# Kernel optimization log

Hardware: AMD Instinct MI355X
Metric: run time of the kernel (lower is better)

## Reference

```python
import jax, jax.numpy as jnp
import numpy as np

TEMPERATURE = 0.07
MSE_WEIGHT = 0.5
SUPCON_WEIGHT = 1.0
EPS = 1e-12  # F.normalize default eps

P_POS = 4000
P_NEG = 4000
NVOX = 32768
FEAT = 128


def setup_inputs() -> dict:
    key = jax.random.key(0)
    k1, k2, k3, k4, k5 = jax.random.split(key, 5)
    Zs = jax.random.normal(k1, (1, FEAT, NVOX), dtype=jnp.float32)
    pos_idx = jax.random.randint(k2, (P_POS,), 0, NVOX, dtype=jnp.int32)
    neg_idx = jax.random.randint(k3, (P_NEG,), 0, NVOX, dtype=jnp.int32)
    feature_diff = jax.random.normal(k4, (1, FEAT, 32, 32, 32), dtype=jnp.float32)
    input_diff = jax.random.normal(k5, (1, FEAT, 32, 32, 32), dtype=jnp.float32)
    return {"Zs": Zs, "pos_idx": pos_idx, "neg_idx": neg_idx,
            "feature_diff": feature_diff, "input_diff": input_diff}


def _l2_normalize_rows(x):
    # F.normalize(x, dim=1): x / max(||x||_2, eps)
    n = jnp.sqrt(jnp.sum(x * x, axis=1, keepdims=True))
    return x / jnp.maximum(n, EPS)


def _supcon_loss(Zs, pos_idx, neg_idx):
    feats = Zs[0].T                                   # [Nvox, F]
    pixels = jnp.concatenate([feats[pos_idx], feats[neg_idx]], axis=0)  # [N, F]
    n = pixels.shape[0]
    labels = jnp.concatenate([jnp.ones((P_POS,), jnp.int32),
                              jnp.zeros((P_NEG,), jnp.int32)])
    pixels = _l2_normalize_rows(pixels)
    dot = jnp.matmul(pixels, pixels.T) / TEMPERATURE  # [N, N]
    dot = _l2_normalize_rows(dot)                     # row-normalize the NxN matrix
    expm = jnp.exp(dot)
    class_mask = (labels[:, None] == labels[None, :]) & ~jnp.eye(n, dtype=bool)
    pos_term = expm * class_mask
    pos_term = jnp.where(pos_term == 0, 1.0, pos_term)
    denom = jnp.sum(expm * ~class_mask, axis=1) - jnp.diagonal(expm)  # [N]
    full_term = jnp.log(pos_term) - jnp.log(denom)[None, :]
    return -(1.0 / n) * jnp.sum(full_term)


def reference(Zs, pos_idx, neg_idx, feature_diff, input_diff):
    supcon = _supcon_loss(Zs, pos_idx, neg_idx)
    mse = jnp.mean((feature_diff - input_diff) ** 2)
    return SUPCON_WEIGHT * supcon + MSE_WEIGHT * mse
```

## Files before the change

kernel.cpp:

```cpp
#include <hip/hip_runtime.h>
#include <hip/hip_bf16.h>
#include <math.h>

typedef unsigned short u16;
typedef float  f32x4  __attribute__((ext_vector_type(4)));
typedef __bf16 bf16x8 __attribute__((ext_vector_type(8)));

#define NPOS   4000
#define NNEG   4000
#define LDP    136
#define TILE_CH 2176
#define MSE_N  4194304

__device__ __forceinline__ void load_lds16(const void* g, void* l) {
  __builtin_amdgcn_global_load_lds(
      (const __attribute__((address_space(1))) unsigned int*)g,
      (__attribute__((address_space(3))) unsigned int*)l, 16, 0, 0);
}

__device__ __forceinline__ float bf2f(u16 h) {
  unsigned u = ((unsigned)h) << 16;
  return __builtin_bit_cast(float, u);
}

__global__ __launch_bounds__(128) void gather_norm_k(
    const float* __restrict__ Zs, const int* __restrict__ pos,
    const int* __restrict__ neg, u16* __restrict__ Pc, u16* __restrict__ Prow) {
  int row = blockIdx.x;
  int f   = threadIdx.x;
  int col = (row < NPOS) ? row : (4096 + row - NPOS);
  int v   = (row < NPOS) ? pos[row] : neg[row - NPOS];
  float x = Zs[((size_t)f << 15) + v];
  float s = x * x;
  #pragma unroll
  for (int o = 1; o < 64; o <<= 1) s += __shfl_xor(s, o, 64);
  __shared__ float red[2];
  if ((f & 63) == 0) red[f >> 6] = s;
  __syncthreads();
  float tot = red[0] + red[1];
  float p = x / fmaxf(sqrtf(tot), 1e-12f);
  __hip_bfloat16 h = __float2bfloat16(p);
  u16 hb = *(u16*)&h;
  Prow[(size_t)col * LDP + f] = hb;
  Pc[(size_t)(col >> 7) * (128 * LDP) + (size_t)f * LDP + (col & 127)] = hb;
}

__global__ __launch_bounds__(256) void gsyrk_k(const u16* __restrict__ Pc,
                                               float* __restrict__ Gpart,
                                               float* __restrict__ S) {
  __shared__ __align__(16) u16 T[128 * LDP];
  int b = blockIdx.x, tid = threadIdx.x;
  int wave = tid >> 6, lane = tid & 63;
  int wm = (wave >> 1) << 6, wn = (wave & 1) << 6;
  int r = lane & 15, q = lane >> 4;
  int sf = tid >> 1, shalf = tid & 1;
  float ssum = 0.f;
  f32x4 acc[4][4];
  #pragma unroll
  for (int a = 0; a < 4; ++a)
    #pragma unroll
    for (int c = 0; c < 4; ++c) {
      acc[a][c][0] = 0.f; acc[a][c][1] = 0.f; acc[a][c][2] = 0.f; acc[a][c][3] = 0.f;
    }
  for (int it = 0; it < 4; ++it) {
    const u16* g = Pc + (size_t)(b * 4 + it) * (128 * LDP);
    #pragma unroll
    for (int k = 0; k < 9; ++k) {
      int cc = k * 256 + tid;
      if (cc < TILE_CH) load_lds16(g + cc * 8, &T[cc * 8]);
    }
    __syncthreads();
    #pragma unroll
    for (int kk = 0; kk < 4; ++kk) {
      int k0 = kk * 32 + q * 8;
      bf16x8 af[4], bfr[4];
      #pragma unroll
      for (int t = 0; t < 4; ++t) {
        af[t]  = *(const bf16x8*)&T[(wm + t * 16 + r) * LDP + k0];
        bfr[t] = *(const bf16x8*)&T[(wn + t * 16 + r) * LDP + k0];
      }
      #pragma unroll
      for (int mt = 0; mt < 4; ++mt)
        #pragma unroll
        for (int nt = 0; nt < 4; ++nt)
          acc[mt][nt] = __builtin_amdgcn_mfma_f32_16x16x32_bf16(
              af[mt], bfr[nt], acc[mt][nt], 0, 0, 0);
    }
    {
      const u16* base = &T[sf * LDP + shalf * 64];
      #pragma unroll
      for (int vb = 0; vb < 8; ++vb) {
        bf16x8 v = *(const bf16x8*)&base[vb * 8];
        #pragma unroll
        for (int j = 0; j < 8; ++j) ssum += (float)v[j];
      }
    }
    __syncthreads();
  }
  float* gp = Gpart + (size_t)b * 16384;
  #pragma unroll
  for (int mt = 0; mt < 4; ++mt)
    #pragma unroll
    for (int nt = 0; nt < 4; ++nt)
      #pragma unroll
      for (int reg = 0; reg < 4; ++reg) {
        int a = wm + mt * 16 + q * 4 + reg;
        int bc = wn + nt * 16 + r;
        gp[a * 128 + bc] = acc[mt][nt][reg];
      }
  ssum += __shfl_xor(ssum, 1, 64);
  if (shalf == 0) atomicAdd(&S[(b >> 3) * 128 + sf], ssum);
}

__global__ __launch_bounds__(256) void reduceG_k(const float* __restrict__ Gpart,
                                                 u16* __restrict__ Gbf) {
  int idx = blockIdx.x * 256 + threadIdx.x;
  int set = idx >> 14, e = idx & 16383;
  float sum = 0.f;
  #pragma unroll
  for (int p = 0; p < 8; ++p) sum += Gpart[(size_t)(set * 8 + p) * 16384 + e];
  __hip_bfloat16 h = __float2bfloat16(sum);
  Gbf[(size_t)set * (128 * LDP) + (size_t)(e >> 7) * LDP + (e & 127)] = *(u16*)&h;
}

__global__ __launch_bounds__(256) void quad_k(
    const u16* __restrict__ Gbf, const u16* __restrict__ Prow,
    const float* __restrict__ Sg, float* __restrict__ qpos, float* __restrict__ qneg,
    float* __restrict__ sdpos, float* __restrict__ sdneg) {
  __shared__ __align__(16) u16 Gs[128 * LDP];
  __shared__ __align__(16) u16 Ps[128 * LDP];
  __shared__ float Sl[256];
  int cb = blockIdx.x, set = blockIdx.y, tid = threadIdx.x;
  Sl[tid] = Sg[tid];
  const u16* gG = Gbf + (size_t)set * (128 * LDP);
  const u16* gP = Prow + (size_t)cb * (128 * LDP);
  #pragma unroll
  for (int k = 0; k < 9; ++k) {
    int cc = k * 256 + tid;
    if (cc < TILE_CH) {
      load_lds16(gG + cc * 8, &Gs[cc * 8]);
      load_lds16(gP + cc * 8, &Ps[cc * 8]);
    }
  }
  __syncthreads();
  int wave = tid >> 6, lane = tid & 63;
  int wm = (wave >> 1) << 6, wn = (wave & 1) << 6;
  int r = lane & 15, q = lane >> 4;
  f32x4 acc[4][4];
  #pragma unroll
  for (int a = 0; a < 4; ++a)
    #pragma unroll
    for (int c = 0; c < 4; ++c) {
      acc[a][c][0] = 0.f; acc[a][c][1] = 0.f; acc[a][c][2] = 0.f; acc[a][c][3] = 0.f;
    }
  #pragma unroll
  for (int kk = 0; kk < 4; ++kk) {
    int k0 = kk * 32 + q * 8;
    bf16x8 af[4], bfr[4];
    #pragma unroll
    for (int t = 0; t < 4; ++t) {
      af[t]  = *(const bf16x8*)&Gs[(wm + t * 16 + r) * LDP + k0];
      bfr[t] = *(const bf16x8*)&Ps[(wn + t * 16 + r) * LDP + k0];
    }
    #pragma unroll
    for (int mt = 0; mt < 4; ++mt)
      #pragma unroll
      for (int nt = 0; nt < 4; ++nt)
        acc[mt][nt] = __builtin_amdgcn_mfma_f32_16x16x32_bf16(
            af[mt], bfr[nt], acc[mt][nt], 0, 0, 0);
  }
  float qv[4] = {0.f, 0.f, 0.f, 0.f};
  #pragma unroll
  for (int nt = 0; nt < 4; ++nt) {
    int il = wn + nt * 16 + r;
    #pragma unroll
    for (int mt = 0; mt < 4; ++mt) {
      const u16* pp = &Ps[il * LDP + wm + mt * 16 + q * 4];
      #pragma unroll
      for (int reg = 0; reg < 4; ++reg)
        qv[nt] += acc[mt][nt][reg] * bf2f(pp[reg]);
    }
  }
  #pragma unroll
  for (int nt = 0; nt < 4; ++nt) {
    qv[nt] += __shfl_xor(qv[nt], 16, 64);
    qv[nt] += __shfl_xor(qv[nt], 32, 64);
  }
  float* qarr = set ? qneg : qpos;
  if (q == 0) {
    #pragma unroll
    for (int nt = 0; nt < 4; ++nt)
      atomicAdd(&qarr[cb * 128 + wn + nt * 16 + r], qv[nt]);
  }
  if (set == 0) {
    int which = tid >> 7, sl = tid & 127;
    const float* Sv = &Sl[which * 128];
    float d = 0.f;
    #pragma unroll
    for (int fb = 0; fb < 16; ++fb) {
      const u16* pv = &Ps[sl * LDP + fb * 8];
      #pragma unroll
      for (int j = 0; j < 8; ++j) d += Sv[fb * 8 + j] * bf2f(pv[j]);
    }
    (which ? sdneg : sdpos)[cb * 128 + sl] = d;
  }
}

__global__ __launch_bounds__(256) void mse_k(const float4* __restrict__ a,
                                             const float4* __restrict__ b,
                                             float* __restrict__ accs) {
  int tid = threadIdx.x;
  float s = 0.f;
  for (size_t idx = (size_t)blockIdx.x * 256 + tid; idx < (MSE_N / 4);
       idx += (size_t)gridDim.x * 256) {
    float4 u = a[idx], w = b[idx];
    float dx = u.x - w.x, dy = u.y - w.y, dz = u.z - w.z, dv = u.w - w.w;
    s += dx * dx + dy * dy + dz * dz + dv * dv;
  }
  #pragma unroll
  for (int o = 1; o < 64; o <<= 1) s += __shfl_xor(s, o, 64);
  __shared__ float red[4];
  if ((tid & 63) == 0) red[tid >> 6] = s;
  __syncthreads();
  if (tid == 0) atomicAdd(&accs[2], red[0] + red[1] + red[2] + red[3]);
}

__global__ __launch_bounds__(1024) void persample_final_k(
    const float* __restrict__ qpos, const float* __restrict__ qneg,
    const float* __restrict__ sdpos, const float* __restrict__ sdneg,
    const float* __restrict__ accs, float* __restrict__ out) {
  int tid = threadIdx.x;
  float lg = 0.f, sm = 0.f;
  for (int col = tid; col < 8192; col += 1024) {
    bool isp = col < NPOS;
    bool isn = (col >= 4096) && (col < 4096 + NNEG);
    if (isp || isn) {
      float qp = qpos[col], qn = qneg[col];
      float c = 1.0f / sqrtf(qp + qn);
      float qo  = isp ? qn : qp;
      float sdo = isp ? sdneg[col] : sdpos[col];
      float sds = isp ? sdpos[col] : sdneg[col];
      float denom = 4000.0f + c * sdo + 0.5f * c * c * qo;
      lg += logf(denom);
      sm += c * (sds - 1.0f);
    }
  }
  #pragma unroll
  for (int o = 1; o < 64; o <<= 1) {
    lg += __shfl_xor(lg, o, 64);
    sm += __shfl_xor(sm, o, 64);
  }
  __shared__ float rl[16], rs[16];
  if ((tid & 63) == 0) { rl[tid >> 6] = lg; rs[tid >> 6] = sm; }
  __syncthreads();
  if (tid == 0) {
    float lgs = 0.f, sms = 0.f;
    #pragma unroll
    for (int w = 0; w < 16; ++w) { lgs += rl[w]; sms += rs[w]; }
    out[0] = lgs - sms * (1.0f / 8000.0f) + 0.5f * (accs[2] * (1.0f / (float)MSE_N));
  }
}

extern "C" void kernel_launch(void* const* d_in, const int* in_sizes, int n_in,
                              void* d_out, int out_size, void* d_ws, size_t ws_size,
                              hipStream_t stream) {
  const float* Zs  = (const float*)d_in[0];
  const int*   pos = (const int*)d_in[1];
  const int*   neg = (const int*)d_in[2];
  const float* fd  = (const float*)d_in[3];
  const float* idf = (const float*)d_in[4];
  float* out = (float*)d_out;

  char* ws = (char*)d_ws;
  u16*   Pc    = (u16*)(ws + 0);
  u16*   Prow  = (u16*)(ws + 2228224);
  float* qpos  = (float*)(ws + 4456448);
  float* qneg  = (float*)(ws + 4489216);
  float* accs  = (float*)(ws + 4521984);
  float* S     = (float*)(ws + 4522048);
  u16*   Gbf   = (u16*)(ws + 4523072);
  float* Gpart = (float*)(ws + 4592704);
  float* sdpos = (float*)(ws + 5641280);
  float* sdneg = (float*)(ws + 5674048);

  hipMemsetAsync(d_ws, 0, 4523072, stream);
  gather_norm_k<<<8000, 128, 0, stream>>>(Zs, pos, neg, Pc, Prow);
  gsyrk_k<<<16, 256, 0, stream>>>(Pc, Gpart, S);
  reduceG_k<<<128, 256, 0, stream>>>(Gpart, Gbf);
  quad_k<<<dim3(64, 2), 256, 0, stream>>>(Gbf, Prow, S, qpos, qneg, sdpos, sdneg);
  mse_k<<<1024, 256, 0, stream>>>((const float4*)fd, (const float4*)idf, accs);
  persample_final_k<<<1, 1024, 0, stream>>>(qpos, qneg, sdpos, sdneg, accs, out);
}
```

Before: 142.6 us.

## Fuse all stages into one cooperative persistent kernel with grid syncs

Replaces six kernel launches with one cooperative kernel of 256 blocks that runs gather/normalize, MSE, Gram partials, the reduction, the quadratic forms and the final loss, separated by grid.sync barriers. The gather now uses one wave per row. The Gram split changes from 16 blocks each covering 4 chunks to 64 blocks covering one chunk each. The memset shrinks to only the accumulators, and the padding columns of Pc are zeroed explicitly. The aim is to remove launch overhead and the large memset, at the cost of grid-wide barriers and of leaving most blocks idle in the later phases.

```diff
diff --git a/kernel.cpp b/kernel.cpp
--- a/kernel.cpp
+++ b/kernel.cpp
@@ -1,13 +1,15 @@
 #include <hip/hip_runtime.h>
 #include <hip/hip_bf16.h>
+#include <hip/hip_cooperative_groups.h>
 #include <math.h>
+
+namespace cg = cooperative_groups;
 
 typedef unsigned short u16;
 typedef float  f32x4  __attribute__((ext_vector_type(4)));
 typedef __bf16 bf16x8 __attribute__((ext_vector_type(8)));
 
 #define NPOS   4000
-#define NNEG   4000
 #define LDP    136
 #define TILE_CH 2176
 #define MSE_N  4194304
@@ -23,61 +25,90 @@
   return __builtin_bit_cast(float, u);
 }
 
-__global__ __launch_bounds__(128) void gather_norm_k(
-    const float* __restrict__ Zs, const int* __restrict__ pos,
-    const int* __restrict__ neg, u16* __restrict__ Pc, u16* __restrict__ Prow) {
-  int row = blockIdx.x;
-  int f   = threadIdx.x;
-  int col = (row < NPOS) ? row : (4096 + row - NPOS);
-  int v   = (row < NPOS) ? pos[row] : neg[row - NPOS];
-  float x = Zs[((size_t)f << 15) + v];
-  float s = x * x;
-  #pragma unroll
-  for (int o = 1; o < 64; o <<= 1) s += __shfl_xor(s, o, 64);
-  __shared__ float red[2];
-  if ((f & 63) == 0) red[f >> 6] = s;
-  __syncthreads();
-  float tot = red[0] + red[1];
-  float p = x / fmaxf(sqrtf(tot), 1e-12f);
-  __hip_bfloat16 h = __float2bfloat16(p);
-  u16 hb = *(u16*)&h;
-  Prow[(size_t)col * LDP + f] = hb;
-  Pc[(size_t)(col >> 7) * (128 * LDP) + (size_t)f * LDP + (col & 127)] = hb;
-}
-
-__global__ __launch_bounds__(256) void gsyrk_k(const u16* __restrict__ Pc,
-                                               float* __restrict__ Gpart,
-                                               float* __restrict__ S) {
-  __shared__ __align__(16) u16 T[128 * LDP];
-  int b = blockIdx.x, tid = threadIdx.x;
+struct FusedArgs {
+  const float* Zs; const int* pos; const int* neg;
+  const float4* fd; const float4* idf;
+  u16* Pc; u16* Prow; float* Gpart; u16* Gbf; float* S;
+  float* qpos; float* qneg; float* sdpos; float* sdneg;
+  float* accs; float* out;
+};
+
+__global__ __launch_bounds__(256) void fused_k(FusedArgs a) {
+  cg::grid_group grid = cg::this_grid();
+  __shared__ __align__(16) u16 T0[128 * LDP];
+  __shared__ __align__(16) u16 T1[128 * LDP];
+  __shared__ float Sl[256];
+  __shared__ float redf[8];
+  int blk = blockIdx.x, tid = threadIdx.x;
   int wave = tid >> 6, lane = tid & 63;
-  int wm = (wave >> 1) << 6, wn = (wave & 1) << 6;
-  int r = lane & 15, q = lane >> 4;
-  int sf = tid >> 1, shalf = tid & 1;
-  float ssum = 0.f;
-  f32x4 acc[4][4];
-  #pragma unroll
-  for (int a = 0; a < 4; ++a)
-    #pragma unroll
-    for (int c = 0; c < 4; ++c) {
-      acc[a][c][0] = 0.f; acc[a][c][1] = 0.f; acc[a][c][2] = 0.f; acc[a][c][3] = 0.f;
-    }
-  for (int it = 0; it < 4; ++it) {
-    const u16* g = Pc + (size_t)(b * 4 + it) * (128 * LDP);
+
+  for (int row = blk * 4 + wave; row < 8000; row += 1024) {
+    int col = (row < NPOS) ? row : (4096 + row - NPOS);
+    int v   = (row < NPOS) ? a.pos[row] : a.neg[row - NPOS];
+    const float* zc = a.Zs + v;
+    float x0 = zc[(size_t)lane << 15];
+    float x1 = zc[(size_t)(lane + 64) << 15];
+    float s = x0 * x0 + x1 * x1;
+    #pragma unroll
+    for (int o = 1; o < 64; o <<= 1) s += __shfl_xor(s, o, 64);
+    float inv = 1.0f / fmaxf(sqrtf(s), 1e-12f);
+    __hip_bfloat16 h0 = __float2bfloat16(x0 * inv);
+    __hip_bfloat16 h1 = __float2bfloat16(x1 * inv);
+    u16 b0 = *(u16*)&h0, b1 = *(u16*)&h1;
+    a.Prow[(size_t)col * LDP + lane]      = b0;
+    a.Prow[(size_t)col * LDP + lane + 64] = b1;
+    size_t cbase = (size_t)(col >> 7) * (128 * LDP) + (col & 127);
+    a.Pc[cbase + (size_t)lane * LDP]        = b0;
+    a.Pc[cbase + (size_t)(lane + 64) * LDP] = b1;
+  }
+  if (blk >= 254) {
+    int ch = (blk == 254) ? 31 : 63;
+    for (int e = tid; e < 128 * 96; e += 256) {
+      int f = e / 96, c = 32 + e % 96;
+      a.Pc[(size_t)ch * (128 * LDP) + (size_t)f * LDP + c] = 0;
+    }
+  }
+  {
+    float ms = 0.f;
+    for (int idx = blk * 256 + tid; idx < MSE_N / 4; idx += 65536) {
+      float4 u = a.fd[idx], w = a.idf[idx];
+      float dx = u.x - w.x, dy = u.y - w.y, dz = u.z - w.z, dv = u.w - w.w;
+      ms += dx * dx + dy * dy + dz * dz + dv * dv;
+    }
+    #pragma unroll
+    for (int o = 1; o < 64; o <<= 1) ms += __shfl_xor(ms, o, 64);
+    if (lane == 0) redf[wave] = ms;
+    __syncthreads();
+    if (tid == 0) atomicAdd(&a.accs[2], redf[0] + redf[1] + redf[2] + redf[3]);
+  }
+  __threadfence();
+  grid.sync();
+
+  if (blk < 64) {
+    const u16* g = a.Pc + (size_t)blk * (128 * LDP);
     #pragma unroll
     for (int k = 0; k < 9; ++k) {
       int cc = k * 256 + tid;
-      if (cc < TILE_CH) load_lds16(g + cc * 8, &T[cc * 8]);
-    }
-    __syncthreads();
+      if (cc < TILE_CH) load_lds16(g + cc * 8, &T0[cc * 8]);
+    }
+    __syncthreads();
+    int wm = (wave >> 1) << 6, wn = (wave & 1) << 6;
+    int r = lane & 15, q = lane >> 4;
+    f32x4 acc[4][4];
+    #pragma unroll
+    for (int x = 0; x < 4; ++x)
+      #pragma unroll
+      for (int y = 0; y < 4; ++y) {
+        acc[x][y][0] = 0.f; acc[x][y][1] = 0.f; acc[x][y][2] = 0.f; acc[x][y][3] = 0.f;
+      }
     #pragma unroll
     for (int kk = 0; kk < 4; ++kk) {
       int k0 = kk * 32 + q * 8;
       bf16x8 af[4], bfr[4];
       #pragma unroll
       for (int t = 0; t < 4; ++t) {
-        af[t]  = *(const bf16x8*)&T[(wm + t * 16 + r) * LDP + k0];
-        bfr[t] = *(const bf16x8*)&T[(wn + t * 16 + r) * LDP + k0];
+        af[t]  = *(const bf16x8*)&T0[(wm + t * 16 + r) * LDP + k0];
+        bfr[t] = *(const bf16x8*)&T0[(wn + t * 16 + r) * LDP + k0];
       }
       #pragma unroll
       for (int mt = 0; mt < 4; ++mt)
@@ -86,208 +117,180 @@
           acc[mt][nt] = __builtin_amdgcn_mfma_f32_16x16x32_bf16(
               af[mt], bfr[nt], acc[mt][nt], 0, 0, 0);
     }
-    {
-      const u16* base = &T[sf * LDP + shalf * 64];
-      #pragma unroll
-      for (int vb = 0; vb < 8; ++vb) {
-        bf16x8 v = *(const bf16x8*)&base[vb * 8];
-        #pragma unroll
-        for (int j = 0; j < 8; ++j) ssum += (float)v[j];
-      }
-    }
-    __syncthreads();
-  }
-  float* gp = Gpart + (size_t)b * 16384;
-  #pragma unroll
-  for (int mt = 0; mt < 4; ++mt)
-    #pragma unroll
-    for (int nt = 0; nt < 4; ++nt)
-      #pragma unroll
-      for (int reg = 0; reg < 4; ++reg) {
-        int a = wm + mt * 16 + q * 4 + reg;
-        int bc = wn + nt * 16 + r;
-        gp[a * 128 + bc] = acc[mt][nt][reg];
-      }
-  ssum += __shfl_xor(ssum, 1, 64);
-  if (shalf == 0) atomicAdd(&S[(b >> 3) * 128 + sf], ssum);
-}
-
-__global__ __launch_bounds__(256) void reduceG_k(const float* __restrict__ Gpart,
-                                                 u16* __restrict__ Gbf) {
-  int idx = blockIdx.x * 256 + threadIdx.x;
-  int set = idx >> 14, e = idx & 16383;
-  float sum = 0.f;
-  #pragma unroll
-  for (int p = 0; p < 8; ++p) sum += Gpart[(size_t)(set * 8 + p) * 16384 + e];
-  __hip_bfloat16 h = __float2bfloat16(sum);
-  Gbf[(size_t)set * (128 * LDP) + (size_t)(e >> 7) * LDP + (e & 127)] = *(u16*)&h;
-}
-
-__global__ __launch_bounds__(256) void quad_k(
-    const u16* __restrict__ Gbf, const u16* __restrict__ Prow,
-    const float* __restrict__ Sg, float* __restrict__ qpos, float* __restrict__ qneg,
-    float* __restrict__ sdpos, float* __restrict__ sdneg) {
-  __shared__ __align__(16) u16 Gs[128 * LDP];
-  __shared__ __align__(16) u16 Ps[128 * LDP];
-  __shared__ float Sl[256];
-  int cb = blockIdx.x, set = blockIdx.y, tid = threadIdx.x;
-  Sl[tid] = Sg[tid];
-  const u16* gG = Gbf + (size_t)set * (128 * LDP);
-  const u16* gP = Prow + (size_t)cb * (128 * LDP);
-  #pragma unroll
-  for (int k = 0; k < 9; ++k) {
-    int cc = k * 256 + tid;
-    if (cc < TILE_CH) {
-      load_lds16(gG + cc * 8, &Gs[cc * 8]);
-      load_lds16(gP + cc * 8, &Ps[cc * 8]);
-    }
-  }
-  __syncthreads();
-  int wave = tid >> 6, lane = tid & 63;
-  int wm = (wave >> 1) << 6, wn = (wave & 1) << 6;
-  int r = lane & 15, q = lane >> 4;
-  f32x4 acc[4][4];
-  #pragma unroll
-  for (int a = 0; a < 4; ++a)
-    #pragma unroll
-    for (int c = 0; c < 4; ++c) {
-      acc[a][c][0] = 0.f; acc[a][c][1] = 0.f; acc[a][c][2] = 0.f; acc[a][c][3] = 0.f;
-    }
-  #pragma unroll
-  for (int kk = 0; kk < 4; ++kk) {
-    int k0 = kk * 32 + q * 8;
-    bf16x8 af[4], bfr[4];
-    #pragma unroll
-    for (int t = 0; t < 4; ++t) {
-      af[t]  = *(const bf16x8*)&Gs[(wm + t * 16 + r) * LDP + k0];
-      bfr[t] = *(const bf16x8*)&Ps[(wn + t * 16 + r) * LDP + k0];
-    }
+    float* gp = a.Gpart + (size_t)blk * 16384;
     #pragma unroll
     for (int mt = 0; mt < 4; ++mt)
       #pragma unroll
       for (int nt = 0; nt < 4; ++nt)
-        acc[mt][nt] = __builtin_amdgcn_mfma_f32_16x16x32_bf16(
-            af[mt], bfr[nt], acc[mt][nt], 0, 0, 0);
-  }
-  float qv[4] = {0.f, 0.f, 0.f, 0.f};
-  #pragma unroll
-  for (int nt = 0; nt < 4; ++nt) {
-    int il = wn + nt * 16 + r;
-    #pragma unroll
-    for (int mt = 0; mt < 4; ++mt) {
-      const u16* pp = &Ps[il * LDP + wm + mt * 16 + q * 4];
-      #pragma unroll
-      for (int reg = 0; reg < 4; ++reg)
-        qv[nt] += acc[mt][nt][reg] * bf2f(pp[reg]);
-    }
-  }
-  #pragma unroll
-  for (int nt = 0; nt < 4; ++nt) {
-    qv[nt] += __shfl_xor(qv[nt], 16, 64);
-    qv[nt] += __shfl_xor(qv[nt], 32, 64);
-  }
-  float* qarr = set ? qneg : qpos;
-  if (q == 0) {
-    #pragma unroll
-    for (int nt = 0; nt < 4; ++nt)
-      atomicAdd(&qarr[cb * 128 + wn + nt * 16 + r], qv[nt]);
-  }
-  if (set == 0) {
-    int which = tid >> 7, sl = tid & 127;
-    const float* Sv = &Sl[which * 128];
-    float d = 0.f;
-    #pragma unroll
-    for (int fb = 0; fb < 16; ++fb) {
-      const u16* pv = &Ps[sl * LDP + fb * 8];
-      #pragma unroll
-      for (int j = 0; j < 8; ++j) d += Sv[fb * 8 + j] * bf2f(pv[j]);
-    }
-    (which ? sdneg : sdpos)[cb * 128 + sl] = d;
-  }
-}
-
-__global__ __launch_bounds__(256) void mse_k(const float4* __restrict__ a,
-                                             const float4* __restrict__ b,
-                                             float* __restrict__ accs) {
-  int tid = threadIdx.x;
-  float s = 0.f;
-  for (size_t idx = (size_t)blockIdx.x * 256 + tid; idx < (MSE_N / 4);
-       idx += (size_t)gridDim.x * 256) {
-    float4 u = a[idx], w = b[idx];
-    float dx = u.x - w.x, dy = u.y - w.y, dz = u.z - w.z, dv = u.w - w.w;
-    s += dx * dx + dy * dy + dz * dz + dv * dv;
-  }
-  #pragma unroll
-  for (int o = 1; o < 64; o <<= 1) s += __shfl_xor(s, o, 64);
-  __shared__ float red[4];
-  if ((tid & 63) == 0) red[tid >> 6] = s;
-  __syncthreads();
-  if (tid == 0) atomicAdd(&accs[2], red[0] + red[1] + red[2] + red[3]);
-}
-
-__global__ __launch_bounds__(1024) void persample_final_k(
-    const float* __restrict__ qpos, const float* __restrict__ qneg,
-    const float* __restrict__ sdpos, const float* __restrict__ sdneg,
-    const float* __restrict__ accs, float* __restrict__ out) {
-  int tid = threadIdx.x;
-  float lg = 0.f, sm = 0.f;
-  for (int col = tid; col < 8192; col += 1024) {
-    bool isp = col < NPOS;
-    bool isn = (col >= 4096) && (col < 4096 + NNEG);
-    if (isp || isn) {
-      float qp = qpos[col], qn = qneg[col];
-      float c = 1.0f / sqrtf(qp + qn);
-      float qo  = isp ? qn : qp;
-      float sdo = isp ? sdneg[col] : sdpos[col];
-      float sds = isp ? sdpos[col] : sdneg[col];
-      float denom = 4000.0f + c * sdo + 0.5f * c * c * qo;
-      lg += logf(denom);
-      sm += c * (sds - 1.0f);
-    }
-  }
-  #pragma unroll
-  for (int o = 1; o < 64; o <<= 1) {
-    lg += __shfl_xor(lg, o, 64);
-    sm += __shfl_xor(sm, o, 64);
-  }
-  __shared__ float rl[16], rs[16];
-  if ((tid & 63) == 0) { rl[tid >> 6] = lg; rs[tid >> 6] = sm; }
-  __syncthreads();
-  if (tid == 0) {
-    float lgs = 0.f, sms = 0.f;
-    #pragma unroll
-    for (int w = 0; w < 16; ++w) { lgs += rl[w]; sms += rs[w]; }
-    out[0] = lgs - sms * (1.0f / 8000.0f) + 0.5f * (accs[2] * (1.0f / (float)MSE_N));
+        #pragma unroll
+        for (int reg = 0; reg < 4; ++reg) {
+          int ar = wm + mt * 16 + q * 4 + reg;
+          int bc = wn + nt * 16 + r;
+          gp[ar * 128 + bc] = acc[mt][nt][reg];
+        }
+    int sf = tid >> 1, sh = tid & 1;
+    const u16* base = &T0[sf * LDP + sh * 64];
+    float ssum = 0.f;
+    #pragma unroll
+    for (int vb = 0; vb < 8; ++vb) {
+      bf16x8 v = *(const bf16x8*)&base[vb * 8];
+      #pragma unroll
+      for (int j = 0; j < 8; ++j) ssum += (float)v[j];
+    }
+    ssum += __shfl_xor(ssum, 1, 64);
+    if (sh == 0) atomicAdd(&a.S[(blk >> 5) * 128 + sf], ssum);
+  }
+  __threadfence();
+  grid.sync();
+
+  if (blk < 128) {
+    int idx = blk * 256 + tid;
+    int set = idx >> 14, e = idx & 16383;
+    float sum = 0.f;
+    #pragma unroll
+    for (int p = 0; p < 32; ++p)
+      sum += a.Gpart[(size_t)(set * 32 + p) * 16384 + e];
+    __hip_bfloat16 h = __float2bfloat16(sum);
+    a.Gbf[(size_t)set * (128 * LDP) + (size_t)(e >> 7) * LDP + (e & 127)] = *(u16*)&h;
+  }
+  __threadfence();
+  grid.sync();
+
+  if (blk < 128) {
+    int cb = blk & 63, set = blk >> 6;
+    Sl[tid] = a.S[tid];
+    const u16* gG = a.Gbf + (size_t)set * (128 * LDP);
+    const u16* gP = a.Prow + (size_t)cb * (128 * LDP);
+    #pragma unroll
+    for (int k = 0; k < 9; ++k) {
+      int cc = k * 256 + tid;
+      if (cc < TILE_CH) {
+        load_lds16(gG + cc * 8, &T0[cc * 8]);
+        load_lds16(gP + cc * 8, &T1[cc * 8]);
+      }
+    }
+    __syncthreads();
+    int wm = (wave >> 1) << 6, wn = (wave & 1) << 6;
+    int r = lane & 15, q = lane >> 4;
+    f32x4 acc[4][4];
+    #pragma unroll
+    for (int x = 0; x < 4; ++x)
+      #pragma unroll
+      for (int y = 0; y < 4; ++y) {
+        acc[x][y][0] = 0.f; acc[x][y][1] = 0.f; acc[x][y][2] = 0.f; acc[x][y][3] = 0.f;
+      }
+    #pragma unroll
+    for (int kk = 0; kk < 4; ++kk) {
+      int k0 = kk * 32 + q * 8;
+      bf16x8 af[4], bfr[4];
+      #pragma unroll
+      for (int t = 0; t < 4; ++t) {
+        af[t]  = *(const bf16x8*)&T0[(wm + t * 16 + r) * LDP + k0];
+        bfr[t] = *(const bf16x8*)&T1[(wn + t * 16 + r) * LDP + k0];
+      }
+      #pragma unroll
+      for (int mt = 0; mt < 4; ++mt)
+        #pragma unroll
+        for (int nt = 0; nt < 4; ++nt)
+          acc[mt][nt] = __builtin_amdgcn_mfma_f32_16x16x32_bf16(
+              af[mt], bfr[nt], acc[mt][nt], 0, 0, 0);
+    }
+    float qv[4] = {0.f, 0.f, 0.f, 0.f};
+    #pragma unroll
+    for (int nt = 0; nt < 4; ++nt) {
+      int il = wn + nt * 16 + r;
+      #pragma unroll
+      for (int mt = 0; mt < 4; ++mt) {
+        const u16* pp = &T1[il * LDP + wm + mt * 16 + q * 4];
+        #pragma unroll
+        for (int reg = 0; reg < 4; ++reg)
+          qv[nt] += acc[mt][nt][reg] * bf2f(pp[reg]);
+      }
+    }
+    #pragma unroll
+    for (int nt = 0; nt < 4; ++nt) {
+      qv[nt] += __shfl_xor(qv[nt], 16, 64);
+      qv[nt] += __shfl_xor(qv[nt], 32, 64);
+    }
+    float* qarr = set ? a.qneg : a.qpos;
+    if (q == 0) {
+      #pragma unroll
+      for (int nt = 0; nt < 4; ++nt)
+        atomicAdd(&qarr[cb * 128 + wn + nt * 16 + r], qv[nt]);
+    }
+    if (set == 0) {
+      int which = tid >> 7, sl = tid & 127;
+      const float* Sv = &Sl[which * 128];
+      float d = 0.f;
+      #pragma unroll
+      for (int fb = 0; fb < 16; ++fb) {
+        const u16* pv = &T1[sl * LDP + fb * 8];
+        #pragma unroll
+        for (int j = 0; j < 8; ++j) d += Sv[fb * 8 + j] * bf2f(pv[j]);
+      }
+      (which ? a.sdneg : a.sdpos)[cb * 128 + sl] = d;
+    }
+  }
+  __threadfence();
+  grid.sync();
+
+  if (blk == 0) {
+    float lg = 0.f, sm = 0.f;
+    for (int col = tid; col < 8192; col += 256) {
+      bool isp = col < NPOS;
+      bool isn = (col >= 4096) && (col < 8096);
+      if (isp || isn) {
+        float qp = a.qpos[col], qn = a.qneg[col];
+        float c = 1.0f / sqrtf(qp + qn);
+        float qo  = isp ? qn : qp;
+        float sdo = isp ? a.sdneg[col] : a.sdpos[col];
+        float sds = isp ? a.sdpos[col] : a.sdneg[col];
+        float denom = 4000.0f + c * sdo + 0.5f * c * c * qo;
+        lg += logf(denom);
+        sm += c * (sds - 1.0f);
+      }
+    }
+    #pragma unroll
+    for (int o = 1; o < 64; o <<= 1) {
+      lg += __shfl_xor(lg, o, 64);
+      sm += __shfl_xor(sm, o, 64);
+    }
+    if (lane == 0) { redf[wave] = lg; redf[4 + wave] = sm; }
+    __syncthreads();
+    if (tid == 0) {
+      float lgs = redf[0] + redf[1] + redf[2] + redf[3];
+      float sms = redf[4] + redf[5] + redf[6] + redf[7];
+      a.out[0] = lgs - sms * (1.0f / 8000.0f)
+               + 0.5f * (a.accs[2] * (1.0f / (float)MSE_N));
+    }
   }
 }
 
 extern "C" void kernel_launch(void* const* d_in, const int* in_sizes, int n_in,
                               void* d_out, int out_size, void* d_ws, size_t ws_size,
                               hipStream_t stream) {
-  const float* Zs  = (const float*)d_in[0];
-  const int*   pos = (const int*)d_in[1];
-  const int*   neg = (const int*)d_in[2];
-  const float* fd  = (const float*)d_in[3];
-  const float* idf = (const float*)d_in[4];
-  float* out = (float*)d_out;
-
   char* ws = (char*)d_ws;
-  u16*   Pc    = (u16*)(ws + 0);
-  u16*   Prow  = (u16*)(ws + 2228224);
-  float* qpos  = (float*)(ws + 4456448);
-  float* qneg  = (float*)(ws + 4489216);
-  float* accs  = (float*)(ws + 4521984);
-  float* S     = (float*)(ws + 4522048);
-  u16*   Gbf   = (u16*)(ws + 4523072);
-  float* Gpart = (float*)(ws + 4592704);
-  float* sdpos = (float*)(ws + 5641280);
-  float* sdneg = (float*)(ws + 5674048);
-
-  hipMemsetAsync(d_ws, 0, 4523072, stream);
-  gather_norm_k<<<8000, 128, 0, stream>>>(Zs, pos, neg, Pc, Prow);
-  gsyrk_k<<<16, 256, 0, stream>>>(Pc, Gpart, S);
-  reduceG_k<<<128, 256, 0, stream>>>(Gpart, Gbf);
-  quad_k<<<dim3(64, 2), 256, 0, stream>>>(Gbf, Prow, S, qpos, qneg, sdpos, sdneg);
-  mse_k<<<1024, 256, 0, stream>>>((const float4*)fd, (const float4*)idf, accs);
-  persample_final_k<<<1, 1024, 0, stream>>>(qpos, qneg, sdpos, sdneg, accs, out);
-}
+  FusedArgs args;
+  args.Zs  = (const float*)d_in[0];
+  args.pos = (const int*)d_in[1];
+  args.neg = (const int*)d_in[2];
+  args.fd  = (const float4*)d_in[3];
+  args.idf = (const float4*)d_in[4];
+  args.out = (float*)d_out;
+
+  args.Pc    = (u16*)(ws + 0);
+  args.Prow  = (u16*)(ws + 2228224);
+  args.Gbf   = (u16*)(ws + 4456448);
+  args.Gpart = (float*)(ws + 4526080);
+  args.sdpos = (float*)(ws + 8720384);
+  args.sdneg = (float*)(ws + 8753152);
+  args.qpos  = (float*)(ws + 8785920);
+  args.qneg  = (float*)(ws + 8818688);
+  args.S     = (float*)(ws + 8851456);
+  args.accs  = (float*)(ws + 8852480);
+
+  hipMemsetAsync(ws + 8785920, 0, 66576, stream);
+
+  void* kargs[] = { &args };
+  hipLaunchCooperativeKernel((void*)fused_k, dim3(256), dim3(256), kargs, 0, stream);
+}
```

Result: slower. 364.6 us (+155.7%).
